# Kernel optimization log

Hardware: AMD Instinct MI355X
Metric: run time of the kernel (lower is better)

Reference implementation:

```python
import jax, jax.numpy as jnp
import numpy as np

B, S, T = 1024, 1024, 32
TAGS = ["O"] + [p + f"T{i}" for i in range(1, 16) for p in ("B-", "I-")] + ["B-T16"]
MASKED = -1.0e4


def _init_params(key):
    bound = float(np.sqrt(6.0 / T))
    k1, k2, k3 = jax.random.split(key, 3)
    start = np.array(jax.random.uniform(k1, (T,), minval=-bound, maxval=bound))
    trans = np.array(jax.random.uniform(k2, (T, T), minval=-bound, maxval=bound))
    end = np.array(jax.random.uniform(k3, (T,), minval=-bound, maxval=bound))
    # structural BIO masking, as in _initialize_parameters
    for i, src in enumerate(TAGS):
        if src.startswith("I-"):
            start[i] = MASKED
        for j, tgt in enumerate(TAGS):
            if (src.startswith("B-") or src.startswith("I-")) and tgt.startswith("I-") and src[2:] != tgt[2:]:
                trans[i, j] = MASKED
            elif src == "O" and tgt.startswith("I-"):
                trans[i, j] = MASKED
    return jnp.asarray(start, jnp.float32), jnp.asarray(trans, jnp.float32), jnp.asarray(end, jnp.float32)


def setup_inputs() -> dict:
    key = jax.random.key(0)
    k_em, k_tag, k_len, k_par = jax.random.split(key, 4)
    emissions = jax.random.normal(k_em, (B, S, T), dtype=jnp.float32)
    tags = jax.random.randint(k_tag, (B, S), 0, T, dtype=jnp.int64) if jax.config.jax_enable_x64 else jax.random.randint(k_tag, (B, S), 0, T).astype(jnp.int32)
    lengths = jax.random.randint(k_len, (B,), S // 4, S + 1)
    mask = jnp.arange(S)[None, :] < lengths[:, None]  # prefix mask, bool [B, S]
    start_transitions, transitions, end_transitions = _init_params(k_par)
    return {
        "emissions": emissions,
        "tags": tags,
        "mask": mask,
        "start_transitions": start_transitions,
        "transitions": transitions,
        "end_transitions": end_transitions,
    }


def reference(emissions, tags, mask, start_transitions, transitions, end_transitions):
    b, s, t = emissions.shape
    ar = jnp.arange(s)
    bidx = jnp.arange(b)
    head = jnp.min(jnp.where(mask, ar[None, :], s - 1), axis=1)  # [B]
    tail = jnp.max(ar[None, :] * mask, axis=1)                   # [B]
    nonempty = mask.sum(axis=1) != 0

    # condition[:, j-1] == (mask[:, j] and head != j), for j = 1..S-1
    cond = mask[:, 1:] & (head[:, None] != ar[None, 1:])  # [B, S-1]

    # ---- numerator (gold path score): additive, fully vectorized ----
    head_tags = tags[bidx, head]
    tail_tags = tags[bidx, tail]
    em_tag = jnp.take_along_axis(emissions, tags[:, :, None], axis=2)[:, :, 0]  # [B, S]
    trans_step = transitions[tags[:, :-1], tags[:, 1:]]                          # [B, S-1]
    numerator = (start_transitions[head_tags]
                 + em_tag[bidx, head]
                 + jnp.sum(jnp.where(cond, trans_step + em_tag[:, 1:], 0.0), axis=1)
                 + end_transitions[tail_tags])
    numerator = jnp.where(nonempty, numerator, 0.0)

    # ---- denominator (log partition): scan over time ----
    score0 = start_transitions[None, :] + emissions[bidx, head]  # [B, T]

    def step(score, xs):
        em_j, cond_j = xs  # [B, T], [B]
        nxt = jax.nn.logsumexp(score[:, :, None] + transitions[None, :, :] + em_j[:, None, :], axis=1)
        return jnp.where(cond_j[:, None], nxt, score), None

    em_seq = jnp.moveaxis(emissions[:, 1:, :], 1, 0)  # [S-1, B, T]
    cond_seq = jnp.moveaxis(cond, 1, 0)               # [S-1, B]
    score_final, _ = jax.lax.scan(step, score0, (em_seq, cond_seq))
    denominator = jax.nn.logsumexp(score_final + end_transitions[None, :], axis=1)
    denominator = jnp.where(nonempty, denominator, 0.0)

    # ---- token_mean reduction ----
    llh = denominator - numerator
    labels = mask.sum(axis=1).astype(emissions.dtype)
    eps = 1e-6
    return jnp.sum(llh / (labels + eps)) / (jnp.sum(labels != 0).astype(emissions.dtype) + eps)
```

## Files before the change

### kernel.cpp

```cpp
#include <hip/hip_runtime.h>
#include <cstdint>

static constexpr int S = 1024;
static constexpr int T = 32;
static constexpr float L2E  = 1.4426950408889634f;
static constexpr float LN2f = 0.6931471805599453f;

typedef __attribute__((ext_vector_type(8)))  short  short8;
typedef __attribute__((ext_vector_type(16))) float  float16;

union Frag { unsigned u[4]; short8 s; };

__global__ void crf_zero(float* ws) {
  ws[0] = 0.0f; ws[1] = 0.0f; ((unsigned*)ws)[2] = 0u;
}

__device__ __forceinline__ float bcast_lane(float v, int k) {
  return __uint_as_float((unsigned)__builtin_amdgcn_readlane((int)__float_as_uint(v), k));
}

__device__ __forceinline__ unsigned cvtpk(float lo, float hi) {
  unsigned r;
  asm("v_cvt_pk_bf16_f32 %0, %1, %2" : "=v"(r) : "v"(lo), "v"(hi));
  return r;
}

__device__ __forceinline__ void gload16(const float* src, float* dst) {
  __builtin_amdgcn_global_load_lds(
      (const __attribute__((address_space(1))) unsigned int*)(src),
      (__attribute__((address_space(3))) unsigned int*)(dst),
      16, 0, 0);
}

__device__ __forceinline__ int sig(int k) {
  int g2 = (k >> 2) & 3;
  if (g2 == 1) g2 = 2; else if (g2 == 2) g2 = 1;
  return (k & ~12) | (g2 << 2);
}

__global__ __launch_bounds__(512, 6) void crf_main(
    const float* __restrict__ em, const int* __restrict__ tags,
    const int* __restrict__ mask, const float* __restrict__ startT,
    const float* __restrict__ trans, const float* __restrict__ endT,
    float* __restrict__ ws, float* __restrict__ out, int B)
{
  __shared__ __align__(16) float    s_g32[8 * 512];
  __shared__ __align__(16) unsigned s_mats[8 * 544];
  __shared__ float s_trans[1024];
  __shared__ short s_tags[1024];
  __shared__ unsigned long long s_mb[17];
  __shared__ int   s_head, s_tail, s_cnt, s_K[8];
  __shared__ float s_num[8];

  const int tid = threadIdx.x;
  const int l   = tid & 63;
  const int wv  = tid >> 6;
  const int b   = blockIdx.x;
  const int n   = l & 31;
  const int h   = l >> 5;

  const float* emb   = em   + (size_t)b * S * T;
  const int*   maskb = mask + (size_t)b * S;
  const int*   tagsb = tags + (size_t)b * S;

  for (int i = tid; i < 1024; i += 512) {
    s_tags[i]  = (short)tagsb[i];
    s_trans[i] = trans[i];
  }
  {
    unsigned long long b0 = __ballot(maskb[wv * 128 + l] != 0);
    unsigned long long b1 = __ballot(maskb[wv * 128 + 64 + l] != 0);
    if (l == 0) { s_mb[2 * wv] = b0; s_mb[2 * wv + 1] = b1; }
    if (tid == 0) s_mb[16] = 0ull;
  }

  Frag Alo, Ahi;
  #pragma unroll
  for (int p = 0; p < 4; ++p) {
    int k0 = 8 * h + 2 * p;
    Alo.u[p] = cvtpk(exp2f(trans[sig(k0 + 0)      * T + n] * L2E),
                     exp2f(trans[sig(k0 + 1)      * T + n] * L2E));
    Ahi.u[p] = cvtpk(exp2f(trans[sig(16 + k0 + 0) * T + n] * L2E),
                     exp2f(trans[sig(16 + k0 + 1) * T + n] * L2E));
  }
  __syncthreads();

  if (wv == 0) {
    int first = 0x7fffffff, last = -1, pc = 0;
    if (l < 16) {
      unsigned long long w = s_mb[l];
      if (w) {
        first = 64 * l + (int)__builtin_ctzll(w);
        last  = 64 * l + 63 - (int)__builtin_clzll(w);
        pc    = (int)__builtin_popcountll(w);
      }
    }
    #pragma unroll
    for (int d = 1; d < 64; d <<= 1) {
      first = min(first, __shfl_xor(first, d));
      last  = max(last,  __shfl_xor(last,  d));
      pc   += __shfl_xor(pc, d);
    }
    if (l == 0) { s_head = first; s_tail = last; s_cnt = pc; }
  }
  __syncthreads();
  const int cnt  = s_cnt;
  const int head = (cnt > 0) ? s_head : 0;
  const int tail = (cnt > 0) ? s_tail : 0;

  const int span = tail - head;
  const int Lc   = (span + 7) >> 3;
  const int c0   = head + 1 + wv * Lc;
  const int c1   = min(c0 + Lc, tail + 1);

  float* bcur = s_g32 + wv * 512;
  float* bnxt = bcur + 256;

  Frag Blo, Bhi;
  #pragma unroll
  for (int p = 0; p < 4; ++p) {
    int k0 = 8 * h + 2 * p;
    Blo.u[p] = ((sig(k0) == n)          ? 0x3F80u : 0u) |
               ((sig(k0 + 1) == n)      ? 0x3F800000u : 0u);
    Bhi.u[p] = ((sig(16 + k0) == n)     ? 0x3F80u : 0u) |
               ((sig(16 + k0 + 1) == n) ? 0x3F800000u : 0u);
  }
  int   Kacc  = 0;
  float numer = 0.0f;
  const float16 Zv = {0,0,0,0,0,0,0,0,0,0,0,0,0,0,0,0};

#define FOLD(JJ, RSC) do {                                                   \
    const float4* gw = (const float4*)(gp + (JJ) * 32);                      \
    float4 wa = gw[h], wb = gw[h + 2], wc = gw[h + 4], wd = gw[h + 6];       \
    float16 D = __builtin_amdgcn_mfma_f32_32x32x16_bf16(Alo.s, Blo.s, Zv, 0, 0, 0); \
    D = __builtin_amdgcn_mfma_f32_32x32x16_bf16(Ahi.s, Bhi.s, D, 0, 0, 0);   \
    D[0]  *= wa.x; D[1]  *= wa.y; D[2]  *= wa.z; D[3]  *= wa.w;              \
    D[4]  *= wb.x; D[5]  *= wb.y; D[6]  *= wb.z; D[7]  *= wb.w;              \
    D[8]  *= wc.x; D[9]  *= wc.y; D[10] *= wc.z; D[11] *= wc.w;              \
    D[12] *= wd.x; D[13] *= wd.y; D[14] *= wd.z; D[15] *= wd.w;              \
    if (RSC) {                                                               \
      float mx = fmaxf(fmaxf(fmaxf(D[0], D[1]), fmaxf(D[2], D[3])),          \
                       fmaxf(fmaxf(D[4], D[5]), fmaxf(D[6], D[7])));         \
      mx = fmaxf(mx, fmaxf(fmaxf(fmaxf(D[8], D[9]),  fmaxf(D[10], D[11])),   \
                           fmaxf(fmaxf(D[12], D[13]), fmaxf(D[14], D[15]))));\
      mx = fmaxf(mx, __shfl_xor(mx, 32));             \
      mx = __uint_as_float((unsigned)__builtin_amdgcn_readfirstlane(         \
               (int)__float_as_uint(mx)));                                   \
      int E = (int)((__float_as_uint(mx) >> 23) & 0xffu);                    \
      float sc = __uint_as_float((unsigned)(254 - E) << 23);                 \
      Kacc += E - 127;                                                       \
      _Pragma("unroll")                                                      \
      for (int q_ = 0; q_ < 16; ++q_) D[q_] *= sc;                           \
    }                                                                        \
    Blo.u[0] = cvtpk(D[0],  D[1]);  Blo.u[1] = cvtpk(D[2],  D[3]);           \
    Blo.u[2] = cvtpk(D[4],  D[5]);  Blo.u[3] = cvtpk(D[6],  D[7]);           \
    Bhi.u[0] = cvtpk(D[8],  D[9]);  Bhi.u[1] = cvtpk(D[10], D[11]);          \
    Bhi.u[2] = cvtpk(D[12], D[13]); Bhi.u[3] = cvtpk(D[14], D[15]);          \
  } while (0)

  if (c0 < c1) {
    const int base = min(c0, S - 8);
    gload16(emb + (size_t)base * T + 4 * l, bcur);
  }

  for (int j0 = c0; j0 < c1; j0 += 8) {
    const int ns   = min(8, c1 - j0);
    const int base = min(j0, S - 8);
    const int d    = j0 - base;

    asm volatile("s_waitcnt vmcnt(0)" ::: "memory");
    {
      float4 r = ((const float4*)bcur)[l];
      r.x = exp2f(r.x * L2E); r.y = exp2f(r.y * L2E);
      r.z = exp2f(r.z * L2E); r.w = exp2f(r.w * L2E);
      ((float4*)bcur)[l] = r;
    }

    if (j0 + 8 < c1) {
      const int nb = min(j0 + 8, S - 8);
      gload16(emb + (size_t)nb * T + 4 * l, bnxt);
    }

    const float* gp = bcur + d * 32;

    const int w = j0 >> 6, o = j0 & 63;
    unsigned long long bits = s_mb[w] >> o;
    if (o) bits |= s_mb[w + 1] << (64 - o);
    unsigned eff = (unsigned)(bits & 0xFFull) & (unsigned)((1u << ns) - 1u);

    if (l < ns && ((eff >> l) & 1u)) {
      int j  = j0 + l;
      int tg = (int)s_tags[j], tp = (int)s_tags[j - 1];
      float gval = gp[l * 32 + tg];
      numer += s_trans[tp * T + tg] + log2f(gval) * LN2f;
    }

    if (eff == 0xFFu) {
      #pragma unroll
      for (int jj = 0; jj < 8; ++jj) FOLD(jj, (jj == 7));
    } else {
      for (int jj = 0; jj < ns; ++jj)
        if ((eff >> jj) & 1u) FOLD(jj, true);
    }

    float* tmp = bcur; bcur = bnxt; bnxt = tmp;
  }
#undef FOLD

  {
    unsigned* mw = s_mats + wv * 544;
    #pragma unroll
    for (int p = 0; p < 4; ++p) {
      mw[(sig(8 * h + 2 * p)      >> 1) * 34 + n] = Blo.u[p];
      mw[(sig(16 + 8 * h + 2 * p) >> 1) * 34 + n] = Bhi.u[p];
    }
  }
  #pragma unroll
  for (int d = 1; d < 64; d <<= 1) numer += __shfl_xor(numer, d);
  if (l == 0) { s_num[wv] = numer; s_K[wv] = Kacc; }
  __syncthreads();

  if (wv == 0) {
    const int t = n;
    const float em0 = emb[head * T + t];
    float sc0 = (startT[t] + em0) * L2E;
    float m0 = sc0;
    #pragma unroll
    for (int d = 1; d < 32; d <<= 1) m0 = fmaxf(m0, __shfl_xor(m0, d));
    float e = exp2f(sc0 - m0);
    float Mtot = m0;

    const unsigned sh = (t & 1) ? 0u : 16u;
    for (int c = 0; c < 8; ++c) {
      const unsigned* mw = s_mats + c * 544 + (t >> 1) * 34;
      float acc = 0.0f;
      #pragma unroll
      for (int q2 = 0; q2 < 16; ++q2) {
        uint2 w2 = *(const uint2*)(mw + 2 * q2);
        float vlo = __uint_as_float((w2.x << sh) & 0xFFFF0000u);
        float vhi = __uint_as_float((w2.y << sh) & 0xFFFF0000u);
        acc = fmaf(vlo, bcast_lane(e, 2 * q2), acc);
        acc = fmaf(vhi, bcast_lane(e, 2 * q2 + 1), acc);
      }
      e = acc;
      Mtot += (float)s_K[c];
      float mx = e;
      #pragma unroll
      for (int d = 1; d < 32; d <<= 1) mx = fmaxf(mx, __shfl_xor(mx, d));
      int E = (int)((__float_as_uint(mx) >> 23) & 0xffu);
      e *= __uint_as_float((unsigned)(254 - E) << 23);
      Mtot += (float)(E - 127);
    }

    float fv = e * exp2f(endT[t] * L2E);
    #pragma unroll
    for (int d = 1; d < 32; d <<= 1) fv += __shfl_xor(fv, d);
    float denom = (Mtot + log2f(fv)) * LN2f;

    if (l == 0) {
      if (cnt > 0) {
        float ntot = 0.0f;
        for (int wq = 0; wq < 8; ++wq) ntot += s_num[wq];
        int th = (int)s_tags[head], tt = (int)s_tags[tail];
        ntot += startT[th] + bcast_lane(em0, th) + endT[tt];
        atomicAdd(&ws[0], (denom - ntot) / ((float)cnt + 1e-6f));
        atomicAdd(&ws[1], 1.0f);
      }
      __threadfence();
      unsigned done = atomicAdd((unsigned*)ws + 2, 1u);
      if (done == (unsigned)(B - 1)) {
        __threadfence();
        out[0] = ws[0] / (ws[1] + 1e-6f);
      }
    }
  }
}

extern "C" void kernel_launch(void* const* d_in, const int* in_sizes, int n_in,
                              void* d_out, int out_size, void* d_ws, size_t ws_size,
                              hipStream_t stream) {
  const float* em     = (const float*)d_in[0];
  const int*   tags   = (const int*)d_in[1];
  const int*   mask   = (const int*)d_in[2];
  const float* startT = (const float*)d_in[3];
  const float* trans  = (const float*)d_in[4];
  const float* endT   = (const float*)d_in[5];
  float* out = (float*)d_out;
  float* ws  = (float*)d_ws;

  const int B = in_sizes[0] / (S * T);

  crf_zero<<<1, 1, 0, stream>>>(ws);
  crf_main<<<B, 512, 0, stream>>>(em, tags, mask, startT, trans, endT, ws, out, B);
}
```

Baseline: 270.6 us.

## Split each wave's chunk into forward and backward matrix chains folded concurrently

Each wave's time chunk is split in half. The first half is folded left-to-right as before, and the second half is folded right-to-left using the transposed transition matrix. The two chains are interleaved per step so two independent MFMA dependency chains overlap, halving the serial chain length. They are combined with one extra matrix product at the end. This doubles the LDS staging buffers and lowers the launch-bounds occupancy hint from 6 to 4, and adds more register pressure and bookkeeping for the reverse window.

After: 272.1 us. No clear change (+0.5%).

```diff
diff --git a/kernel.cpp b/kernel.cpp
--- a/kernel.cpp
+++ b/kernel.cpp
@@ -38,13 +38,13 @@
   return (k & ~12) | (g2 << 2);
 }
 
-__global__ __launch_bounds__(512, 6) void crf_main(
+__global__ __launch_bounds__(512, 4) void crf_main(
     const float* __restrict__ em, const int* __restrict__ tags,
     const int* __restrict__ mask, const float* __restrict__ startT,
     const float* __restrict__ trans, const float* __restrict__ endT,
     float* __restrict__ ws, float* __restrict__ out, int B)
 {
-  __shared__ __align__(16) float    s_g32[8 * 512];
+  __shared__ __align__(16) float    s_g32[8 * 1024];
   __shared__ __align__(16) unsigned s_mats[8 * 544];
   __shared__ float s_trans[1024];
   __shared__ short s_tags[1024];
@@ -74,14 +74,18 @@
     if (tid == 0) s_mb[16] = 0ull;
   }
 
-  Frag Alo, Ahi;
+  Frag A1lo, A1hi, A2lo, A2hi;
   #pragma unroll
   for (int p = 0; p < 4; ++p) {
     int k0 = 8 * h + 2 * p;
-    Alo.u[p] = cvtpk(exp2f(trans[sig(k0 + 0)      * T + n] * L2E),
-                     exp2f(trans[sig(k0 + 1)      * T + n] * L2E));
-    Ahi.u[p] = cvtpk(exp2f(trans[sig(16 + k0 + 0) * T + n] * L2E),
-                     exp2f(trans[sig(16 + k0 + 1) * T + n] * L2E));
+    A1lo.u[p] = cvtpk(exp2f(trans[sig(k0 + 0)      * T + n] * L2E),
+                      exp2f(trans[sig(k0 + 1)      * T + n] * L2E));
+    A1hi.u[p] = cvtpk(exp2f(trans[sig(16 + k0 + 0) * T + n] * L2E),
+                      exp2f(trans[sig(16 + k0 + 1) * T + n] * L2E));
+    A2lo.u[p] = cvtpk(exp2f(trans[n * T + sig(k0 + 0)] * L2E),
+                      exp2f(trans[n * T + sig(k0 + 1)] * L2E));
+    A2hi.u[p] = cvtpk(exp2f(trans[n * T + sig(16 + k0 + 0)] * L2E),
+                      exp2f(trans[n * T + sig(16 + k0 + 1)] * L2E));
   }
   __syncthreads();
 
@@ -112,9 +116,12 @@
   const int Lc   = (span + 7) >> 3;
   const int c0   = head + 1 + wv * Lc;
   const int c1   = min(c0 + Lc, tail + 1);
-
-  float* bcur = s_g32 + wv * 512;
-  float* bnxt = bcur + 256;
+  const int cm   = c0 + ((max(c1 - c0, 0) + 1) >> 1);
+  const int len1 = cm - c0;
+  const int nw   = (len1 + 7) >> 3;
+
+  float* w1 = s_g32 + wv * 1024;
+  float* w2 = w1 + 512;
 
   Frag Blo, Bhi;
   #pragma unroll
@@ -125,87 +132,181 @@
     Bhi.u[p] = ((sig(16 + k0) == n)     ? 0x3F80u : 0u) |
                ((sig(16 + k0 + 1) == n) ? 0x3F800000u : 0u);
   }
+  float16 D2;
+  #pragma unroll
+  for (int q = 0; q < 16; ++q)
+    D2[q] = (((q & 3) + 8 * (q >> 2) + 4 * h) == n) ? 1.0f : 0.0f;
+
   int   Kacc  = 0;
   float numer = 0.0f;
   const float16 Zv = {0,0,0,0,0,0,0,0,0,0,0,0,0,0,0,0};
 
-#define FOLD(JJ, RSC) do {                                                   \
-    const float4* gw = (const float4*)(gp + (JJ) * 32);                      \
+#define RESCALE16(DV) do {                                                   \
+    float mx_ = fmaxf(fmaxf(fmaxf(DV[0], DV[1]), fmaxf(DV[2], DV[3])),       \
+                      fmaxf(fmaxf(DV[4], DV[5]), fmaxf(DV[6], DV[7])));      \
+    mx_ = fmaxf(mx_, fmaxf(fmaxf(fmaxf(DV[8], DV[9]),  fmaxf(DV[10], DV[11])),\
+                           fmaxf(fmaxf(DV[12], DV[13]), fmaxf(DV[14], DV[15]))));\
+    mx_ = fmaxf(mx_, __shfl_xor(mx_, 32));   \
+    mx_ = __uint_as_float((unsigned)__builtin_amdgcn_readfirstlane(          \
+              (int)__float_as_uint(mx_)));                                   \
+    int E_ = (int)((__float_as_uint(mx_) >> 23) & 0xffu);                    \
+    float sc_ = __uint_as_float((unsigned)(254 - E_) << 23);                 \
+    Kacc += E_ - 127;                                                        \
+    _Pragma("unroll")                                                        \
+    for (int q_ = 0; q_ < 16; ++q_) DV[q_] *= sc_;                           \
+  } while (0)
+
+#define FOLD1(JJ, RSC) do {                                                  \
+    const float4* gw = (const float4*)(gp1 + (JJ) * 32);                     \
     float4 wa = gw[h], wb = gw[h + 2], wc = gw[h + 4], wd = gw[h + 6];       \
-    float16 D = __builtin_amdgcn_mfma_f32_32x32x16_bf16(Alo.s, Blo.s, Zv, 0, 0, 0); \
-    D = __builtin_amdgcn_mfma_f32_32x32x16_bf16(Ahi.s, Bhi.s, D, 0, 0, 0);   \
+    float16 D = __builtin_amdgcn_mfma_f32_32x32x16_bf16(A1lo.s, Blo.s, Zv, 0, 0, 0); \
+    D = __builtin_amdgcn_mfma_f32_32x32x16_bf16(A1hi.s, Bhi.s, D, 0, 0, 0);  \
     D[0]  *= wa.x; D[1]  *= wa.y; D[2]  *= wa.z; D[3]  *= wa.w;              \
     D[4]  *= wb.x; D[5]  *= wb.y; D[6]  *= wb.z; D[7]  *= wb.w;              \
     D[8]  *= wc.x; D[9]  *= wc.y; D[10] *= wc.z; D[11] *= wc.w;              \
     D[12] *= wd.x; D[13] *= wd.y; D[14] *= wd.z; D[15] *= wd.w;              \
-    if (RSC) {                                                               \
-      float mx = fmaxf(fmaxf(fmaxf(D[0], D[1]), fmaxf(D[2], D[3])),          \
-                       fmaxf(fmaxf(D[4], D[5]), fmaxf(D[6], D[7])));         \
-      mx = fmaxf(mx, fmaxf(fmaxf(fmaxf(D[8], D[9]),  fmaxf(D[10], D[11])),   \
-                           fmaxf(fmaxf(D[12], D[13]), fmaxf(D[14], D[15]))));\
-      mx = fmaxf(mx, __shfl_xor(mx, 32));             \
-      mx = __uint_as_float((unsigned)__builtin_amdgcn_readfirstlane(         \
-               (int)__float_as_uint(mx)));                                   \
-      int E = (int)((__float_as_uint(mx) >> 23) & 0xffu);                    \
-      float sc = __uint_as_float((unsigned)(254 - E) << 23);                 \
-      Kacc += E - 127;                                                       \
-      _Pragma("unroll")                                                      \
-      for (int q_ = 0; q_ < 16; ++q_) D[q_] *= sc;                           \
-    }                                                                        \
+    if (RSC) RESCALE16(D);                                                   \
     Blo.u[0] = cvtpk(D[0],  D[1]);  Blo.u[1] = cvtpk(D[2],  D[3]);           \
     Blo.u[2] = cvtpk(D[4],  D[5]);  Blo.u[3] = cvtpk(D[6],  D[7]);           \
     Bhi.u[0] = cvtpk(D[8],  D[9]);  Bhi.u[1] = cvtpk(D[10], D[11]);          \
     Bhi.u[2] = cvtpk(D[12], D[13]); Bhi.u[3] = cvtpk(D[14], D[15]);          \
   } while (0)
 
-  if (c0 < c1) {
-    const int base = min(c0, S - 8);
-    gload16(emb + (size_t)base * T + 4 * l, bcur);
-  }
-
-  for (int j0 = c0; j0 < c1; j0 += 8) {
-    const int ns   = min(8, c1 - j0);
-    const int base = min(j0, S - 8);
-    const int d    = j0 - base;
+#define FOLD2(JJ, RSC) do {                                                  \
+    const float4* gw = (const float4*)(gp2 + (JJ) * 32);                     \
+    float4 wa = gw[h], wb = gw[h + 2], wc = gw[h + 4], wd = gw[h + 6];       \
+    D2[0]  *= wa.x; D2[1]  *= wa.y; D2[2]  *= wa.z; D2[3]  *= wa.w;          \
+    D2[4]  *= wb.x; D2[5]  *= wb.y; D2[6]  *= wb.z; D2[7]  *= wb.w;          \
+    D2[8]  *= wc.x; D2[9]  *= wc.y; D2[10] *= wc.z; D2[11] *= wc.w;          \
+    D2[12] *= wd.x; D2[13] *= wd.y; D2[14] *= wd.z; D2[15] *= wd.w;          \
+    if (RSC) RESCALE16(D2);                                                  \
+    Frag t2lo, t2hi;                                                         \
+    t2lo.u[0] = cvtpk(D2[0],  D2[1]);  t2lo.u[1] = cvtpk(D2[2],  D2[3]);     \
+    t2lo.u[2] = cvtpk(D2[4],  D2[5]);  t2lo.u[3] = cvtpk(D2[6],  D2[7]);     \
+    t2hi.u[0] = cvtpk(D2[8],  D2[9]);  t2hi.u[1] = cvtpk(D2[10], D2[11]);    \
+    t2hi.u[2] = cvtpk(D2[12], D2[13]); t2hi.u[3] = cvtpk(D2[14], D2[15]);    \
+    float16 Dn_ = __builtin_amdgcn_mfma_f32_32x32x16_bf16(A2lo.s, t2lo.s, Zv, 0, 0, 0); \
+    D2 = __builtin_amdgcn_mfma_f32_32x32x16_bf16(A2hi.s, t2hi.s, Dn_, 0, 0, 0); \
+  } while (0)
+
+  if (nw > 0) {
+    gload16(emb + (size_t)min(c0, S - 8) * T + 4 * l, w1);
+    if (c1 > cm) gload16(emb + (size_t)max(c1 - 8, 0) * T + 4 * l, w2);
+  }
+
+  for (int i = 0; i < nw; ++i) {
+    const int pp  = (i & 1) << 8;
+    float* w1c = w1 + pp;
+    float* w2c = w2 + pp;
+
+    const int bf   = c0 + 8 * i;
+    const int lb1  = min(bf, S - 8);
+    const int d1   = bf - lb1;
+    const int hi1  = min(8, cm - bf);
+
+    const int jhi  = c1 - 8 * i;
+    const bool ron = (jhi > cm);
+    const int lb2  = max(jhi - 8, 0);
+    const int klo2 = max(cm - lb2, 0);
+    const int khi2 = jhi - lb2;
 
     asm volatile("s_waitcnt vmcnt(0)" ::: "memory");
     {
-      float4 r = ((const float4*)bcur)[l];
+      float4 r = ((const float4*)w1c)[l];
       r.x = exp2f(r.x * L2E); r.y = exp2f(r.y * L2E);
       r.z = exp2f(r.z * L2E); r.w = exp2f(r.w * L2E);
-      ((float4*)bcur)[l] = r;
-    }
-
-    if (j0 + 8 < c1) {
-      const int nb = min(j0 + 8, S - 8);
-      gload16(emb + (size_t)nb * T + 4 * l, bnxt);
-    }
-
-    const float* gp = bcur + d * 32;
-
-    const int w = j0 >> 6, o = j0 & 63;
-    unsigned long long bits = s_mb[w] >> o;
-    if (o) bits |= s_mb[w + 1] << (64 - o);
-    unsigned eff = (unsigned)(bits & 0xFFull) & (unsigned)((1u << ns) - 1u);
-
-    if (l < ns && ((eff >> l) & 1u)) {
-      int j  = j0 + l;
+      ((float4*)w1c)[l] = r;
+    }
+    if (ron) {
+      float4 r = ((const float4*)w2c)[l];
+      r.x = exp2f(r.x * L2E); r.y = exp2f(r.y * L2E);
+      r.z = exp2f(r.z * L2E); r.w = exp2f(r.w * L2E);
+      ((float4*)w2c)[l] = r;
+    }
+
+    if (i + 1 < nw) {
+      const int npp = pp ^ 256;
+      gload16(emb + (size_t)min(c0 + 8 * (i + 1), S - 8) * T + 4 * l, w1 + npp);
+      const int njhi = c1 - 8 * (i + 1);
+      if (njhi > cm)
+        gload16(emb + (size_t)max(njhi - 8, 0) * T + 4 * l, w2 + npp);
+    }
+
+    const float* gp1 = w1c + d1 * 32;
+    const float* gp2 = w2c;
+
+    unsigned eff1;
+    {
+      const int wdi = bf >> 6, o = bf & 63;
+      unsigned long long bits = s_mb[wdi] >> o;
+      if (o) bits |= s_mb[wdi + 1] << (64 - o);
+      eff1 = (unsigned)(bits & 0xFFull) & (unsigned)((1u << hi1) - 1u);
+    }
+    unsigned eff2 = 0u;
+    if (ron) {
+      const int wdi = lb2 >> 6, o = lb2 & 63;
+      unsigned long long bits = s_mb[wdi] >> o;
+      if (o) bits |= s_mb[wdi + 1] << (64 - o);
+      eff2 = (unsigned)(bits & 0xFFull) &
+             (unsigned)((1u << khi2) - (1u << klo2));
+    }
+
+    if (l < 8 && ((eff1 >> l) & 1u)) {
+      int j = bf + l;
       int tg = (int)s_tags[j], tp = (int)s_tags[j - 1];
-      float gval = gp[l * 32 + tg];
-      numer += s_trans[tp * T + tg] + log2f(gval) * LN2f;
-    }
-
-    if (eff == 0xFFu) {
-      #pragma unroll
-      for (int jj = 0; jj < 8; ++jj) FOLD(jj, (jj == 7));
+      numer += s_trans[tp * T + tg] + log2f(gp1[l * 32 + tg]) * LN2f;
+    }
+    if (l < 8 && ((eff2 >> l) & 1u)) {
+      int j = lb2 + l;
+      int tg = (int)s_tags[j], tp = (int)s_tags[j - 1];
+      numer += s_trans[tp * T + tg] + log2f(gp2[l * 32 + tg]) * LN2f;
+    }
+
+    if (eff1 == 0xFFu && eff2 == 0xFFu) {
+      FOLD1(0, false); FOLD2(7, false);
+      FOLD1(1, false); FOLD2(6, false);
+      FOLD1(2, false); FOLD2(5, false);
+      FOLD1(3, false); FOLD2(4, false);
+      FOLD1(4, false); FOLD2(3, false);
+      FOLD1(5, false); FOLD2(2, false);
+      FOLD1(6, false); FOLD2(1, false);
+      FOLD1(7, true);  FOLD2(0, true);
     } else {
-      for (int jj = 0; jj < ns; ++jj)
-        if ((eff >> jj) & 1u) FOLD(jj, true);
-    }
-
-    float* tmp = bcur; bcur = bnxt; bnxt = tmp;
-  }
-#undef FOLD
+      if (eff1 == 0xFFu) {
+        FOLD1(0, false); FOLD1(1, false); FOLD1(2, false); FOLD1(3, false);
+        FOLD1(4, false); FOLD1(5, false); FOLD1(6, false); FOLD1(7, true);
+      } else {
+        for (int jj = 0; jj < hi1; ++jj)
+          if ((eff1 >> jj) & 1u) FOLD1(jj, true);
+      }
+      if (eff2 == 0xFFu) {
+        FOLD2(7, false); FOLD2(6, false); FOLD2(5, false); FOLD2(4, false);
+        FOLD2(3, false); FOLD2(2, false); FOLD2(1, false); FOLD2(0, true);
+      } else if (ron) {
+        for (int jj = khi2 - 1; jj >= klo2; --jj)
+          if ((eff2 >> jj) & 1u) FOLD2(jj, true);
+      }
+    }
+  }
+#undef FOLD1
+#undef FOLD2
+
+  RESCALE16(D2);
+  {
+    Frag Z2lo, Z2hi;
+    Z2lo.u[0] = cvtpk(D2[0],  D2[1]);  Z2lo.u[1] = cvtpk(D2[2],  D2[3]);
+    Z2lo.u[2] = cvtpk(D2[4],  D2[5]);  Z2lo.u[3] = cvtpk(D2[6],  D2[7]);
+    Z2hi.u[0] = cvtpk(D2[8],  D2[9]);  Z2hi.u[1] = cvtpk(D2[10], D2[11]);
+    Z2hi.u[2] = cvtpk(D2[12], D2[13]); Z2hi.u[3] = cvtpk(D2[14], D2[15]);
+    float16 Dc = __builtin_amdgcn_mfma_f32_32x32x16_bf16(Z2lo.s, Blo.s, Zv, 0, 0, 0);
+    Dc = __builtin_amdgcn_mfma_f32_32x32x16_bf16(Z2hi.s, Bhi.s, Dc, 0, 0, 0);
+    RESCALE16(Dc);
+    Blo.u[0] = cvtpk(Dc[0],  Dc[1]);  Blo.u[1] = cvtpk(Dc[2],  Dc[3]);
+    Blo.u[2] = cvtpk(Dc[4],  Dc[5]);  Blo.u[3] = cvtpk(Dc[6],  Dc[7]);
+    Bhi.u[0] = cvtpk(Dc[8],  Dc[9]);  Bhi.u[1] = cvtpk(Dc[10], Dc[11]);
+    Bhi.u[2] = cvtpk(Dc[12], Dc[13]); Bhi.u[3] = cvtpk(Dc[14], Dc[15]);
+  }
+#undef RESCALE16
 
   {
     unsigned* mw = s_mats + wv * 544;
```
